# Optimization experiments

Hardware: AMD Instinct MI355X
Metric: run time of the kernel (lower is better)

The kernel has to match this reference:

```python
import jax, jax.numpy as jnp
import numpy as np

N, E = 100000, 1600000
NODE_IN, EDGE_IN, H = 128, 16, 128


def sage_conv(x, src, dst, Wl, Wr, b, n_nodes):
    # PyG SAGEConv (aggr='mean'): out = lin_l(mean_{j->i} x_j) + lin_r(x_i), bias on lin_l
    msg_sum = jax.ops.segment_sum(x[src], dst, num_segments=n_nodes)      # [N, d]
    cnt = jax.ops.segment_sum(jnp.ones((src.shape[0],), x.dtype), dst, num_segments=n_nodes)
    mean = msg_sum / jnp.maximum(cnt, 1.0)[:, None]                        # empty neighborhoods -> 0
    return mean @ Wl + x @ Wr + b


def setup_inputs() -> dict:
    key = jax.random.key(0)
    ks = jax.random.split(key, 12)
    s = lambda d: 1.0 / np.sqrt(d)
    return {
        "x": jax.random.normal(ks[0], (N, NODE_IN), jnp.float32),
        "edge_index": jax.random.randint(ks[1], (2, E), 0, N, dtype=jnp.int64),
        "edge_attr": jax.random.normal(ks[2], (E, EDGE_IN), jnp.float32),
        "Wl1": jax.random.normal(ks[3], (NODE_IN, H), jnp.float32) * s(NODE_IN),
        "Wr1": jax.random.normal(ks[4], (NODE_IN, H), jnp.float32) * s(NODE_IN),
        "b1": jnp.zeros((H,), jnp.float32),
        "Wl2": jax.random.normal(ks[5], (H, H), jnp.float32) * s(H),
        "Wr2": jax.random.normal(ks[6], (H, H), jnp.float32) * s(H),
        "b2": jnp.zeros((H,), jnp.float32),
        "Wm1": jax.random.normal(ks[7], (2 * H + EDGE_IN, H), jnp.float32) * s(2 * H + EDGE_IN),
        "bm1": jnp.zeros((H,), jnp.float32),
        "Wm2": jax.random.normal(ks[8], (H, 1), jnp.float32) * s(H),
        "bm2": jnp.zeros((1,), jnp.float32),
    }


def reference(x, edge_index, edge_attr, Wl1, Wr1, b1, Wl2, Wr2, b2, Wm1, bm1, Wm2, bm2):
    src, dst = edge_index[0], edge_index[1]
    h = jax.nn.relu(sage_conv(x, src, dst, Wl1, Wr1, b1, N))
    h = jax.nn.relu(sage_conv(h, src, dst, Wl2, Wr2, b2, N))
    edge_feat = jnp.concatenate([h[src], h[dst], edge_attr], axis=1)  # [E, 2H+edge_in]
    out = jax.nn.relu(edge_feat @ Wm1 + bm1) @ Wm2 + bm2               # dropout is identity in eval
    return out.reshape(-1)
```

## Files before the change

kernel.cpp:

```cpp
#include <hip/hip_runtime.h>

typedef _Float16 f16;
typedef _Float16 f16x2 __attribute__((ext_vector_type(2)));
typedef _Float16 f16x8 __attribute__((ext_vector_type(8)));
typedef float f32x4 __attribute__((ext_vector_type(4)));

#define MFMA16(a,b,c) __builtin_amdgcn_mfma_f32_16x16x32_f16((a),(b),(c),0,0,0)

__global__ void k_detect(const long long* ei, int n_nodes, int* flag) {
    long long v = ei[threadIdx.x];
    int bad = (v < 0 || v >= n_nodes);
    unsigned long long m = __ballot(bad);
    if (threadIdx.x == 0) *flag = (m == 0ULL);
}

__global__ void k_idx(const void* ei, int E, const int* __restrict__ flag,
                      int* __restrict__ src, int* __restrict__ dst,
                      int* __restrict__ deg) {
    int e = blockIdx.x * 256 + threadIdx.x;
    if (e >= E) return;
    int s, d;
    if (*flag) {
        const long long* p = (const long long*)ei;
        s = (int)p[e];
        d = (int)p[(size_t)E + e];
    } else {
        const int* p = (const int*)ei;
        s = p[e];
        d = p[(size_t)E + e];
    }
    src[e] = s;
    dst[e] = d;
    atomicAdd(&deg[d], 1);
}

__global__ void k_x2h(const float* __restrict__ x, f16* __restrict__ xh, int n) {
    int i = (blockIdx.x * 256 + threadIdx.x) * 8;
    if (i >= n) return;
    float4 a = *(const float4*)(x + i);
    float4 b = *(const float4*)(x + i + 4);
    f16x8 h;
    h[0] = (f16)a.x; h[1] = (f16)a.y; h[2] = (f16)a.z; h[3] = (f16)a.w;
    h[4] = (f16)b.x; h[5] = (f16)b.y; h[6] = (f16)b.z; h[7] = (f16)b.w;
    *(f16x8*)(xh + i) = h;
}

__global__ void k_wfrag(const float* __restrict__ Wa, const float* __restrict__ Wb,
                        f16* __restrict__ dst, int KS) {
    int t = blockIdx.x * 256 + threadIdx.x;
    int total = KS * 8 * 64;
    if (t >= total) return;
    int l = t & 63;
    int s = t >> 9;
    int k0 = s * 32 + (l >> 4) * 8;
    int j = ((t >> 6) & 7) * 16 + (l & 15);
    f16x8 h;
    #pragma unroll
    for (int e = 0; e < 8; e++) {
        int k = k0 + e;
        float v = (k < 128) ? Wa[k * 128 + j] : Wb[(k - 128) * 128 + j];
        h[e] = (f16)v;
    }
    *(f16x8*)(dst + (size_t)t * 8) = h;
}

__global__ void k_zfrag(const float* __restrict__ Wm1, f16* __restrict__ dst) {
    int t = blockIdx.x * 256 + threadIdx.x;
    if (t >= 4 * 16 * 64) return;
    int lane = t & 63, c = (t >> 6) & 15, s = t >> 10;
    int k0 = s * 32 + (lane >> 4) * 8;
    int j = c * 16 + (lane & 15);
    f16x8 h;
    #pragma unroll
    for (int e = 0; e < 8; e++) {
        int k = k0 + e;
        float v = (j < 128) ? Wm1[k * 128 + j] : Wm1[(128 + k) * 128 + (j - 128)];
        h[e] = (f16)v;
    }
    *(f16x8*)(dst + (size_t)t * 8) = h;
}

__global__ void k_wefrag(const float* __restrict__ Wm1, f16* __restrict__ dst) {
    int t = blockIdx.x * 256 + threadIdx.x;
    if (t >= 8 * 64) return;
    int lane = t & 63, ct = t >> 6;
    int k0 = (lane >> 4) * 8;
    int j = (ct >> 1) * 32 + 2 * (lane & 15) + (ct & 1);
    f16x8 h;
    #pragma unroll
    for (int e = 0; e < 8; e++) {
        int k = k0 + e;
        h[e] = (k < 16) ? (f16)Wm1[(256 + k) * 128 + j] : (f16)0.0f;
    }
    *(f16x8*)(dst + (size_t)t * 8) = h;
}

__global__ void k_bsum(const int* __restrict__ deg, int n, int* __restrict__ bsum) {
    __shared__ int ws[4];
    const int tid = threadIdx.x;
    int i = blockIdx.x * 1024 + tid * 4;
    int s = 0;
    if (i + 3 < n) {
        int4 d = *(const int4*)(deg + i);
        s = d.x + d.y + d.z + d.w;
    } else {
        #pragma unroll
        for (int j = 0; j < 4; j++) if (i + j < n) s += deg[i + j];
    }
    #pragma unroll
    for (int m = 1; m < 64; m <<= 1) s += __shfl_xor(s, m, 64);
    if ((tid & 63) == 0) ws[tid >> 6] = s;
    __syncthreads();
    if (tid == 0) bsum[blockIdx.x] = ws[0] + ws[1] + ws[2] + ws[3];
}

__global__ void k_bscan(int* __restrict__ bsum, int nb, int* __restrict__ rowptr_n) {
    __shared__ int wsum[4];
    const int tid = threadIdx.x, lane = tid & 63, wid = tid >> 6;
    int v = (tid < nb) ? bsum[tid] : 0;
    int inc = v;
    #pragma unroll
    for (int off = 1; off < 64; off <<= 1) {
        int u = __shfl_up(inc, off, 64);
        if (lane >= off) inc += u;
    }
    if (lane == 63) wsum[wid] = inc;
    __syncthreads();
    int woff = 0;
    for (int j = 0; j < wid; j++) woff += wsum[j];
    int excl = woff + inc - v;
    if (tid < nb) bsum[tid] = excl;
    if (tid == nb - 1) rowptr_n[0] = excl + v;
}

__global__ void k_rowptr(const int* __restrict__ deg, int n, const int* __restrict__ boff,
                         int* __restrict__ rowptr, int* __restrict__ cursor) {
    __shared__ int wsum[4];
    const int tid = threadIdx.x, lane = tid & 63, wid = tid >> 6;
    int i = blockIdx.x * 1024 + tid * 4;
    int d0 = 0, d1 = 0, d2 = 0, d3 = 0;
    if (i + 3 < n) {
        int4 d = *(const int4*)(deg + i);
        d0 = d.x; d1 = d.y; d2 = d.z; d3 = d.w;
    } else {
        if (i     < n) d0 = deg[i];
        if (i + 1 < n) d1 = deg[i + 1];
        if (i + 2 < n) d2 = deg[i + 2];
        if (i + 3 < n) d3 = deg[i + 3];
    }
    int s = d0 + d1 + d2 + d3;
    int inc = s;
    #pragma unroll
    for (int off = 1; off < 64; off <<= 1) {
        int u = __shfl_up(inc, off, 64);
        if (lane >= off) inc += u;
    }
    if (lane == 63) wsum[wid] = inc;
    __syncthreads();
    int woff = 0;
    for (int j = 0; j < wid; j++) woff += wsum[j];
    int excl = boff[blockIdx.x] + woff + inc - s;
    int e1 = excl + d0, e2 = e1 + d1, e3 = e2 + d2;
    if (i     < n) { rowptr[i]     = excl; cursor[i]     = excl; }
    if (i + 1 < n) { rowptr[i + 1] = e1;   cursor[i + 1] = e1; }
    if (i + 2 < n) { rowptr[i + 2] = e2;   cursor[i + 2] = e2; }
    if (i + 3 < n) { rowptr[i + 3] = e3;   cursor[i + 3] = e3; }
}

__global__ void k_scatter(const int* __restrict__ src, const int* __restrict__ dst, int E,
                          int* __restrict__ cursor, int* __restrict__ col,
                          int* __restrict__ eid, int* __restrict__ dstp) {
    int e = blockIdx.x * 256 + threadIdx.x;
    if (e < E) {
        int d = dst[e];
        int p = atomicAdd(&cursor[d], 1);
        col[p] = src[e];
        eid[p] = e;
        dstp[p] = d;
    }
}

#define AP 136
template<int DO_Z>
__global__ __launch_bounds__(256, DO_Z ? 4 : 5) void k_fuse(
    const f16* __restrict__ tab,
    const int* __restrict__ rowptr, const int* __restrict__ col,
    const f16* __restrict__ Wf, const float* __restrict__ bias,
    const f16* __restrict__ zwf, const float* __restrict__ bm1,
    f16* __restrict__ out, int n_rows) {
    __shared__ __align__(16) f16 sA[64 * AP];
    const int tid = threadIdx.x, lane = tid & 63, w = tid >> 6;
    const int l15 = lane & 15, g = lane >> 4;
    const int base = blockIdx.x * 64;

    const int g16 = tid >> 4, c = tid & 15;
    #pragma unroll
    for (int rep = 0; rep < 4; rep++) {
        const int node = base + rep * 16 + g16;
        float acc[8] = {0.f, 0.f, 0.f, 0.f, 0.f, 0.f, 0.f, 0.f};
        int d = 1;
        if (node < n_rows) {
            const int s0 = rowptr[node], s1 = rowptr[node + 1];
            int k = s0;
            for (; k + 3 < s1; k += 4) {
                const int n0 = col[k], n1 = col[k + 1], n2 = col[k + 2], n3 = col[k + 3];
                f16x8 v0 = *(const f16x8*)(tab + (size_t)n0 * 128 + c * 8);
                f16x8 v1 = *(const f16x8*)(tab + (size_t)n1 * 128 + c * 8);
                f16x8 v2 = *(const f16x8*)(tab + (size_t)n2 * 128 + c * 8);
                f16x8 v3 = *(const f16x8*)(tab + (size_t)n3 * 128 + c * 8);
                #pragma unroll
                for (int j = 0; j < 8; j++)
                    acc[j] += ((float)v0[j] + (float)v1[j]) + ((float)v2[j] + (float)v3[j]);
            }
            for (; k < s1; ++k) {
                const int n0 = col[k];
                f16x8 v0 = *(const f16x8*)(tab + (size_t)n0 * 128 + c * 8);
                #pragma unroll
                for (int j = 0; j < 8; j++) acc[j] += (float)v0[j];
            }
            d = s1 - s0; if (d < 1) d = 1;
        }
        const float inv = 1.f / (float)d;
        f16x8 r;
        #pragma unroll
        for (int j = 0; j < 8; j++) r[j] = (f16)(acc[j] * inv);
        *(f16x8*)&sA[(rep * 16 + g16) * AP + c * 8] = r;
    }
    __syncthreads();

    const int c0 = (2 * w) * 16 + l15, c1 = c0 + 16;
    const float b0 = bias[c0], b1 = bias[c1];
    f32x4 acc[4][2];
    #pragma unroll
    for (int t = 0; t < 4; t++) {
        acc[t][0] = f32x4{b0, b0, b0, b0};
        acc[t][1] = f32x4{b1, b1, b1, b1};
    }
    #pragma unroll
    for (int s = 0; s < 8; s++) {
        f16x8 bf0 = *(const f16x8*)&Wf[((size_t)(s * 8 + 2 * w    ) * 64 + lane) * 8];
        f16x8 bf1 = *(const f16x8*)&Wf[((size_t)(s * 8 + 2 * w + 1) * 64 + lane) * 8];
        const int koff = (s & 3) * 32 + g * 8;
        #pragma unroll
        for (int t = 0; t < 4; t++) {
            f16x8 a;
            if (s < 4) {
                a = *(const f16x8*)&sA[(t * 16 + l15) * AP + koff];
            } else {
                int row = base + t * 16 + l15;
                if (row >= n_rows) row = n_rows - 1;
                a = *(const f16x8*)(tab + (size_t)row * 128 + koff);
            }
            acc[t][0] = MFMA16(a, bf0, acc[t][0]);
            acc[t][1] = MFMA16(a, bf1, acc[t][1]);
        }
    }

    if (DO_Z == 0) {
        #pragma unroll
        for (int t = 0; t < 4; t++) {
            #pragma unroll
            for (int i = 0; i < 4; i++) {
                int row = base + t * 16 + g * 4 + i;
                if (row < n_rows) {
                    float v0 = acc[t][0][i]; v0 = v0 > 0.f ? v0 : 0.f;
                    float v1 = acc[t][1][i]; v1 = v1 > 0.f ? v1 : 0.f;
                    out[(size_t)row * 128 + c0] = (f16)v0;
                    out[(size_t)row * 128 + c1] = (f16)v1;
                }
            }
        }
    } else {
        __syncthreads();
        #pragma unroll
        for (int t = 0; t < 4; t++) {
            #pragma unroll
            for (int i = 0; i < 4; i++) {
                const int rl = t * 16 + g * 4 + i;
                float v0 = acc[t][0][i]; v0 = v0 > 0.f ? v0 : 0.f;
                float v1 = acc[t][1][i]; v1 = v1 > 0.f ? v1 : 0.f;
                sA[rl * AP + c0] = (f16)v0;
                sA[rl * AP + c1] = (f16)v1;
            }
        }
        __syncthreads();
        #pragma unroll
        for (int half = 0; half < 2; half++) {
            const int j0 = (4 * w + 2 * half) * 16 + l15, j1 = j0 + 16;
            const float zb0 = (j0 >= 128) ? bm1[j0 - 128] : 0.0f;
            const float zb1 = (j1 >= 128) ? bm1[j1 - 128] : 0.0f;
            f32x4 zacc[4][2];
            #pragma unroll
            for (int t = 0; t < 4; t++) {
                zacc[t][0] = f32x4{zb0, zb0, zb0, zb0};
                zacc[t][1] = f32x4{zb1, zb1, zb1, zb1};
            }
            #pragma unroll
            for (int s = 0; s < 4; s++) {
                f16x8 wf0 = *(const f16x8*)&zwf[((size_t)(s * 16 + 4 * w + 2 * half    ) * 64 + lane) * 8];
                f16x8 wf1 = *(const f16x8*)&zwf[((size_t)(s * 16 + 4 * w + 2 * half + 1) * 64 + lane) * 8];
                const int koff = s * 32 + g * 8;
                #pragma unroll
                for (int t = 0; t < 4; t++) {
                    f16x8 a = *(const f16x8*)&sA[(t * 16 + l15) * AP + koff];
                    zacc[t][0] = MFMA16(a, wf0, zacc[t][0]);
                    zacc[t][1] = MFMA16(a, wf1, zacc[t][1]);
                }
            }
            #pragma unroll
            for (int t = 0; t < 4; t++) {
                #pragma unroll
                for (int i = 0; i < 4; i++) {
                    int row = base + t * 16 + g * 4 + i;
                    if (row < n_rows) {
                        out[(size_t)row * 256 + j0] = (f16)zacc[t][0][i];
                        out[(size_t)row * 256 + j1] = (f16)zacc[t][1][i];
                    }
                }
            }
        }
    }
}

#define ZP 136
__global__ __launch_bounds__(256, 4) void k_edge2(
    const f16* __restrict__ z, const float* __restrict__ ea,
    const int* __restrict__ colp, const int* __restrict__ dstp, const int* __restrict__ eidp,
    const f16* __restrict__ wef, const float* __restrict__ Wm2,
    const float* __restrict__ bm2, float* __restrict__ tmp,
    int E, int iters, int gridW) {
    __shared__ __align__(16) f16 sZ[64 * ZP];
    __shared__ __align__(16) f16 sEA[4 * 64 * 8];
    __shared__ float sPart[4][64];
    const int tid = threadIdx.x, lane = tid & 63, w = tid >> 6;
    const int l15 = lane & 15, g = lane >> 4;
    const int sr = lane >> 2, sq = lane & 3;
    const int slot_s = w * 16 + sr;

    for (int i = tid; i < 4 * 64; i += 256)
        *(f16x8*)(&sEA[0] + (size_t)i * 8) = f16x8{};

    const f16x8 be0 = *(const f16x8*)(wef + ((size_t)((2 * w) * 64 + lane)) * 8);
    const f16x8 be1 = *(const f16x8*)(wef + ((size_t)((2 * w + 1) * 64 + lane)) * 8);
    const int cp = w * 32 + 2 * l15;
    const float2 w2v = *(const float2*)&Wm2[cp];
    const float bv = bm2[0];

    f16x8 zs[4], zd[4];
    union { f16 h[4]; uint2 u2; } eh;

    auto stage_load = [&](int pbase) {
        int pr = pbase + slot_s; if (pr > E - 1) pr = E - 1;
        const int is = colp[pr], id = dstp[pr], ee = eidp[pr];
        const f16* ps = z + (size_t)is * 256 + sq * 8;
        const f16* pd = z + (size_t)id * 256 + 128 + sq * 8;
        #pragma unroll
        for (int i = 0; i < 4; i++) {
            zs[i] = *(const f16x8*)(ps + i * 32);
            zd[i] = *(const f16x8*)(pd + i * 32);
        }
        float4 ev = *(const float4*)(ea + (size_t)ee * 16 + sq * 4);
        eh.h[0] = (f16)ev.x; eh.h[1] = (f16)ev.y; eh.h[2] = (f16)ev.z; eh.h[3] = (f16)ev.w;
    };
    auto stage_write = [&]() {
        f16* zp = &sZ[0] + slot_s * ZP + sq * 8;
        #pragma unroll
        for (int i = 0; i < 4; i++) {
            f16x8 v = zs[i] + zd[i];
            *(f16x8*)(zp + i * 32) = v;
        }
        f16* ep = &sEA[0] +
                  ((size_t)((slot_s >> 4) * 64 + (sq >> 1) * 16 + (slot_s & 15)) * 8 + (sq & 1) * 4);
        *(uint2*)ep = eh.u2;
    };

    stage_load(blockIdx.x * 64);
    __syncthreads();
    stage_write();
    __syncthreads();

    for (int it = 0; it < iters; ++it) {
        const int pbase = (blockIdx.x + it * gridW) * 64;
        if (pbase >= E) break;
        const int nxt = (blockIdx.x + (it + 1) * gridW) * 64;
        const bool has_next = (it + 1 < iters) && (nxt < E);
        if (has_next) stage_load(nxt);

        f32x4 acc[4][2];
        #pragma unroll
        for (int t = 0; t < 4; t++) { acc[t][0] = f32x4{0,0,0,0}; acc[t][1] = f32x4{0,0,0,0}; }
        #pragma unroll
        for (int t = 0; t < 4; t++) {
            f16x8 a = *(const f16x8*)(&sEA[0] + ((size_t)(t * 64 + lane)) * 8);
            acc[t][0] = MFMA16(a, be0, acc[t][0]);
            acc[t][1] = MFMA16(a, be1, acc[t][1]);
        }
        #pragma unroll
        for (int t = 0; t < 4; t++) {
            float p[4];
            #pragma unroll
            for (int i = 0; i < 4; i++) {
                int slot = t * 16 + g * 4 + i;
                f16x2 zz = *(const f16x2*)&sZ[slot * ZP + cp];
                float v0 = (float)zz[0] + acc[t][0][i]; v0 = v0 > 0.f ? v0 : 0.f;
                float v1 = (float)zz[1] + acc[t][1][i]; v1 = v1 > 0.f ? v1 : 0.f;
                p[i] = v0 * w2v.x + v1 * w2v.y;
            }
            #pragma unroll
            for (int m = 1; m < 16; m <<= 1)
                #pragma unroll
                for (int i = 0; i < 4; i++) p[i] += __shfl_xor(p[i], m, 64);
            if (l15 == 0)
                #pragma unroll
                for (int i = 0; i < 4; i++) sPart[w][t * 16 + g * 4 + i] = p[i];
        }
        __syncthreads();
        if (tid < 64) {
            int p = pbase + tid;
            if (p < E)
                tmp[p] = sPart[0][tid] + sPart[1][tid] + sPart[2][tid] + sPart[3][tid] + bv;
        }
        if (has_next) stage_write();
        __syncthreads();
    }
}

__global__ void k_perm(const float* __restrict__ tmp, const int* __restrict__ eidp,
                       float* __restrict__ out, int E) {
    int p = blockIdx.x * 256 + threadIdx.x;
    if (p < E) out[eidp[p]] = tmp[p];
}

extern "C" void kernel_launch(void* const* d_in, const int* in_sizes, int n_in,
                              void* d_out, int out_size, void* d_ws, size_t ws_size,
                              hipStream_t stream) {
    const float* x   = (const float*)d_in[0];
    const void*  ei  = d_in[1];
    const float* ea  = (const float*)d_in[2];
    const float* Wl1 = (const float*)d_in[3];
    const float* Wr1 = (const float*)d_in[4];
    const float* b1  = (const float*)d_in[5];
    const float* Wl2 = (const float*)d_in[6];
    const float* Wr2 = (const float*)d_in[7];
    const float* b2  = (const float*)d_in[8];
    const float* Wm1 = (const float*)d_in[9];
    const float* bm1 = (const float*)d_in[10];
    const float* Wm2 = (const float*)d_in[11];
    const float* bm2 = (const float*)d_in[12];

    const int N = in_sizes[0] / 128;
    const int E = in_sizes[1] / 2;

    char* ws = (char*)d_ws;
    size_t off = 0;
    auto alloc = [&](size_t bytes) -> void* {
        void* p = ws + off;
        off = (off + bytes + 255) & ~(size_t)255;
        return p;
    };
    f16* z      = (f16*)alloc((size_t)N * 256 * 2);
    f16* xh     = z;
    f16* h1     = (f16*)alloc((size_t)N * 128 * 2);
    int* src    = (int*)alloc((size_t)E * 4);
    int* dst    = (int*)alloc((size_t)E * 4);
    int* col    = (int*)alloc((size_t)E * 4);
    int* eid    = (int*)alloc((size_t)E * 4);
    int* dstp   = (int*)alloc((size_t)E * 4);
    float* tmp  = (float*)alloc((size_t)E * 4);
    int* deg    = (int*)alloc((size_t)N * 4);
    int* rowptr = (int*)alloc((size_t)(N + 1) * 4);
    int* cursor = (int*)alloc((size_t)N * 4);
    int* bsum   = (int*)alloc((size_t)1024 * 4);
    f16* w1f    = (f16*)alloc((size_t)8 * 8 * 64 * 8 * 2);
    f16* w2f    = (f16*)alloc((size_t)8 * 8 * 64 * 8 * 2);
    f16* zwf    = (f16*)alloc((size_t)4 * 16 * 64 * 8 * 2);
    f16* wef    = (f16*)alloc((size_t)8 * 64 * 8 * 2);
    int* flag   = (int*)alloc(4);
    if (off > ws_size) return;

    const int eb = (E + 255) / 256;
    const int nbk = (N + 1023) / 1024;
    const int rb64 = (N + 63) / 64;

    k_detect<<<1, 64, 0, stream>>>((const long long*)ei, N, flag);
    hipMemsetAsync(deg, 0, (size_t)N * 4, stream);
    k_idx<<<eb, 256, 0, stream>>>(ei, E, flag, src, dst, deg);
    k_x2h<<<(N * 128 / 8 + 255) / 256, 256, 0, stream>>>(x, xh, N * 128);
    k_wfrag<<<16, 256, 0, stream>>>(Wl1, Wr1, w1f, 8);
    k_wfrag<<<16, 256, 0, stream>>>(Wl2, Wr2, w2f, 8);
    k_zfrag<<<16, 256, 0, stream>>>(Wm1, zwf);
    k_wefrag<<<2, 256, 0, stream>>>(Wm1, wef);

    k_bsum<<<nbk, 256, 0, stream>>>(deg, N, bsum);
    k_bscan<<<1, 256, 0, stream>>>(bsum, nbk, rowptr + N);
    k_rowptr<<<nbk, 256, 0, stream>>>(deg, N, bsum, rowptr, cursor);
    k_scatter<<<eb, 256, 0, stream>>>(src, dst, E, cursor, col, eid, dstp);

    k_fuse<0><<<rb64, 256, 0, stream>>>(xh, rowptr, col, w1f, b1, nullptr, nullptr, h1, N);
    k_fuse<1><<<rb64, 256, 0, stream>>>(h1, rowptr, col, w2f, b2, zwf, bm1, z, N);

    const int eg = 1792;
    const int nb = (E + 63) / 64;
    const int e_iters = (nb + eg - 1) / eg;
    k_edge2<<<eg, 256, 0, stream>>>(z, ea, col, dstp, eid, wef, Wm2, bm2,
                                    tmp, E, e_iters, eg);
    k_perm<<<eb, 256, 0, stream>>>(tmp, eid, (float*)d_out, E);
}
```

Before: 530.4 us.

## Make edge MLP kernel wave-independent with per-wave 16-edge tiles

```diff
diff --git a/kernel.cpp b/kernel.cpp
--- a/kernel.cpp
+++ b/kernel.cpp
@@ -322,106 +322,109 @@
     }
 }
 
-#define ZP 136
-__global__ __launch_bounds__(256, 4) void k_edge2(
+#define ZP3 136
+__global__ __launch_bounds__(256, 4) void k_edge3(
     const f16* __restrict__ z, const float* __restrict__ ea,
     const int* __restrict__ colp, const int* __restrict__ dstp, const int* __restrict__ eidp,
     const f16* __restrict__ wef, const float* __restrict__ Wm2,
     const float* __restrict__ bm2, float* __restrict__ tmp,
-    int E, int iters, int gridW) {
-    __shared__ __align__(16) f16 sZ[64 * ZP];
-    __shared__ __align__(16) f16 sEA[4 * 64 * 8];
-    __shared__ float sPart[4][64];
+    int E, int iters, int nwaves) {
+    __shared__ __align__(16) f16 sZ[4][16 * ZP3];
     const int tid = threadIdx.x, lane = tid & 63, w = tid >> 6;
     const int l15 = lane & 15, g = lane >> 4;
-    const int sr = lane >> 2, sq = lane & 3;
-    const int slot_s = w * 16 + sr;
-
-    for (int i = tid; i < 4 * 64; i += 256)
-        *(f16x8*)(&sEA[0] + (size_t)i * 8) = f16x8{};
-
-    const f16x8 be0 = *(const f16x8*)(wef + ((size_t)((2 * w) * 64 + lane)) * 8);
-    const f16x8 be1 = *(const f16x8*)(wef + ((size_t)((2 * w + 1) * 64 + lane)) * 8);
-    const int cp = w * 32 + 2 * l15;
-    const float2 w2v = *(const float2*)&Wm2[cp];
+    const int te = lane >> 2, sq = lane & 3;
+    const int gw = blockIdx.x * 4 + w;
+
+    f16x8 be[8];
+    #pragma unroll
+    for (int cc = 0; cc < 8; cc++)
+        be[cc] = *(const f16x8*)(wef + ((size_t)(cc * 64 + lane)) * 8);
+    float2 w2p[4];
+    #pragma unroll
+    for (int pg = 0; pg < 4; pg++)
+        w2p[pg] = *(const float2*)&Wm2[pg * 32 + 2 * l15];
     const float bv = bm2[0];
 
+    f16* myZ = &sZ[w][0];
+
     f16x8 zs[4], zd[4];
-    union { f16 h[4]; uint2 u2; } eh;
-
-    auto stage_load = [&](int pbase) {
-        int pr = pbase + slot_s; if (pr > E - 1) pr = E - 1;
-        const int is = colp[pr], id = dstp[pr], ee = eidp[pr];
+    f16x8 a_cur, a_next;
+
+    auto stage_load = [&](int pbase, f16x8* zsv, f16x8* zdv, f16x8& av) {
+        int pr = pbase + te; if (pr > E - 1) pr = E - 1;
+        const int is = colp[pr], id = dstp[pr];
         const f16* ps = z + (size_t)is * 256 + sq * 8;
         const f16* pd = z + (size_t)id * 256 + 128 + sq * 8;
         #pragma unroll
         for (int i = 0; i < 4; i++) {
-            zs[i] = *(const f16x8*)(ps + i * 32);
-            zd[i] = *(const f16x8*)(pd + i * 32);
-        }
-        float4 ev = *(const float4*)(ea + (size_t)ee * 16 + sq * 4);
-        eh.h[0] = (f16)ev.x; eh.h[1] = (f16)ev.y; eh.h[2] = (f16)ev.z; eh.h[3] = (f16)ev.w;
+            zsv[i] = *(const f16x8*)(ps + i * 32);
+            zdv[i] = *(const f16x8*)(pd + i * 32);
+        }
+        int pe = pbase + l15; if (pe > E - 1) pe = E - 1;
+        f16x8 av_ = {};
+        if (g < 2) {
+            const int ee = eidp[pe];
+            float4 e0 = *(const float4*)(ea + (size_t)ee * 16 + g * 8);
+            float4 e1 = *(const float4*)(ea + (size_t)ee * 16 + g * 8 + 4);
+            av_[0] = (f16)e0.x; av_[1] = (f16)e0.y; av_[2] = (f16)e0.z; av_[3] = (f16)e0.w;
+            av_[4] = (f16)e1.x; av_[5] = (f16)e1.y; av_[6] = (f16)e1.z; av_[7] = (f16)e1.w;
+        }
+        av = av_;
     };
     auto stage_write = [&]() {
-        f16* zp = &sZ[0] + slot_s * ZP + sq * 8;
+        f16* zp = myZ + te * ZP3 + sq * 8;
         #pragma unroll
         for (int i = 0; i < 4; i++) {
             f16x8 v = zs[i] + zd[i];
             *(f16x8*)(zp + i * 32) = v;
         }
-        f16* ep = &sEA[0] +
-                  ((size_t)((slot_s >> 4) * 64 + (sq >> 1) * 16 + (slot_s & 15)) * 8 + (sq & 1) * 4);
-        *(uint2*)ep = eh.u2;
     };
 
-    stage_load(blockIdx.x * 64);
-    __syncthreads();
+    stage_load(gw * 16, zs, zd, a_cur);
     stage_write();
-    __syncthreads();
 
     for (int it = 0; it < iters; ++it) {
-        const int pbase = (blockIdx.x + it * gridW) * 64;
+        const int pbase = (gw + it * nwaves) * 16;
         if (pbase >= E) break;
-        const int nxt = (blockIdx.x + (it + 1) * gridW) * 64;
+        const int nxt = (gw + (it + 1) * nwaves) * 16;
         const bool has_next = (it + 1 < iters) && (nxt < E);
-        if (has_next) stage_load(nxt);
-
-        f32x4 acc[4][2];
-        #pragma unroll
-        for (int t = 0; t < 4; t++) { acc[t][0] = f32x4{0,0,0,0}; acc[t][1] = f32x4{0,0,0,0}; }
-        #pragma unroll
-        for (int t = 0; t < 4; t++) {
-            f16x8 a = *(const f16x8*)(&sEA[0] + ((size_t)(t * 64 + lane)) * 8);
-            acc[t][0] = MFMA16(a, be0, acc[t][0]);
-            acc[t][1] = MFMA16(a, be1, acc[t][1]);
-        }
-        #pragma unroll
-        for (int t = 0; t < 4; t++) {
-            float p[4];
+        if (has_next) stage_load(nxt, zs, zd, a_next);
+
+        f32x4 acc[8];
+        #pragma unroll
+        for (int cc = 0; cc < 8; cc++) acc[cc] = f32x4{0.f, 0.f, 0.f, 0.f};
+        #pragma unroll
+        for (int cc = 0; cc < 8; cc++) acc[cc] = MFMA16(a_cur, be[cc], acc[cc]);
+
+        float p[4];
+        #pragma unroll
+        for (int i = 0; i < 4; i++) {
+            const int edge = g * 4 + i;
+            float s = 0.f;
+            #pragma unroll
+            for (int pg = 0; pg < 4; pg++) {
+                f16x2 zz = *(const f16x2*)&myZ[edge * ZP3 + pg * 32 + 2 * l15];
+                float v0 = (float)zz[0] + acc[2 * pg    ][i]; v0 = v0 > 0.f ? v0 : 0.f;
+                float v1 = (float)zz[1] + acc[2 * pg + 1][i]; v1 = v1 > 0.f ? v1 : 0.f;
+                s += v0 * w2p[pg].x + v1 * w2p[pg].y;
+            }
+            p[i] = s;
+        }
+        #pragma unroll
+        for (int m = 1; m < 16; m <<= 1)
+            #pragma unroll
+            for (int i = 0; i < 4; i++) p[i] += __shfl_xor(p[i], m, 64);
+        if (l15 == 0) {
             #pragma unroll
             for (int i = 0; i < 4; i++) {
-                int slot = t * 16 + g * 4 + i;
-                f16x2 zz = *(const f16x2*)&sZ[slot * ZP + cp];
-                float v0 = (float)zz[0] + acc[t][0][i]; v0 = v0 > 0.f ? v0 : 0.f;
-                float v1 = (float)zz[1] + acc[t][1][i]; v1 = v1 > 0.f ? v1 : 0.f;
-                p[i] = v0 * w2v.x + v1 * w2v.y;
-            }
-            #pragma unroll
-            for (int m = 1; m < 16; m <<= 1)
-                #pragma unroll
-                for (int i = 0; i < 4; i++) p[i] += __shfl_xor(p[i], m, 64);
-            if (l15 == 0)
-                #pragma unroll
-                for (int i = 0; i < 4; i++) sPart[w][t * 16 + g * 4 + i] = p[i];
-        }
-        __syncthreads();
-        if (tid < 64) {
-            int p = pbase + tid;
-            if (p < E)
-                tmp[p] = sPart[0][tid] + sPart[1][tid] + sPart[2][tid] + sPart[3][tid] + bv;
-        }
-        if (has_next) stage_write();
-        __syncthreads();
+                int pp = pbase + g * 4 + i;
+                if (pp < E) tmp[pp] = p[i] + bv;
+            }
+        }
+        if (has_next) {
+            stage_write();
+            a_cur = a_next;
+        }
     }
 }
 
@@ -500,9 +503,10 @@
     k_fuse<1><<<rb64, 256, 0, stream>>>(h1, rowptr, col, w2f, b2, zwf, bm1, z, N);
 
     const int eg = 1792;
-    const int nb = (E + 63) / 64;
-    const int e_iters = (nb + eg - 1) / eg;
-    k_edge2<<<eg, 256, 0, stream>>>(z, ea, col, dstp, eid, wef, Wm2, bm2,
-                                    tmp, E, e_iters, eg);
+    const int nwaves = eg * 4;
+    const int ntiles = (E + 15) / 16;
+    const int e_iters = (ntiles + nwaves - 1) / nwaves;
+    k_edge3<<<eg, 256, 0, stream>>>(z, ea, col, dstp, eid, wef, Wm2, bm2,
+                                    tmp, E, e_iters, nwaves);
     k_perm<<<eb, 256, 0, stream>>>(tmp, eid, (float*)d_out, E);
 }
```

Result: faster. 502.6 us (-5.2%).
